# Kernel tuning notes

Measured on AMD Instinct MI355X. Metric: run time of the kernel, lower is better.

Reference implementation:

```python
import jax, jax.numpy as jnp
import numpy as np

N_POINTS = 1_000_000
NUM_PILLARS = 30_000
BN_EPS = 1e-3


def _bn(x, gamma, beta, mean, var):
    # eval-mode BatchNorm1d with eps=0.001
    return (x - mean) * (gamma * jax.lax.rsqrt(var + BN_EPS)) + beta


def setup_inputs() -> dict:
    key = jax.random.key(0)
    ks = jax.random.split(key, 5)
    C1, C2 = 32, 64
    return {
        "points": jax.random.normal(ks[0], (N_POINTS, 5), dtype=jnp.float32),
        "f_center": jax.random.normal(ks[1], (N_POINTS, 3), dtype=jnp.float32),
        "unq_inv": jax.random.randint(ks[2], (N_POINTS,), 0, NUM_PILLARS, dtype=jnp.int32),
        "W1": jax.random.normal(ks[3], (7, C1), dtype=jnp.float32) * 0.1,
        "g1": jnp.ones((C1,), jnp.float32),
        "b1": jnp.zeros((C1,), jnp.float32),
        "m1": jnp.zeros((C1,), jnp.float32),
        "v1": jnp.ones((C1,), jnp.float32),
        "W2": jax.random.normal(ks[4], (C2, C1), dtype=jnp.float32) * 0.1,
        "g2": jnp.ones((C1,), jnp.float32),
        "b2": jnp.zeros((C1,), jnp.float32),
        "m2": jnp.zeros((C1,), jnp.float32),
        "v2": jnp.ones((C1,), jnp.float32),
    }


def reference(points, f_center, unq_inv, W1, g1, b1, m1, v1, W2, g2, b2, m2, v2):
    # gen_feat: concat(f_center, points[:,1:]) -> Linear(no bias) -> BN -> ReLU
    feats = jnp.concatenate([f_center, points[:, 1:]], axis=-1)  # [N, 7]
    h = jnp.maximum(_bn(feats @ W1, g1, b1, m1, v1), 0.0)        # [N, 32]

    # scatter_mean over pillars, then gather back and concat
    seg_sum = jax.ops.segment_sum(h, unq_inv, num_segments=NUM_PILLARS)
    counts = jax.ops.segment_sum(jnp.ones((h.shape[0],), h.dtype), unq_inv,
                                 num_segments=NUM_PILLARS)
    seg_mean = seg_sum / jnp.maximum(counts, 1.0)[:, None]       # [P, 32]
    h2 = jnp.concatenate([h, seg_mean[unq_inv]], axis=1)         # [N, 64]

    # AVFEO: Linear(64,32,no bias) -> BN -> ReLU
    out_fc = jnp.maximum(_bn(h2 @ W2, g2, b2, m2, v2), 0.0)      # [N, 32]

    # scatter_max over pillars (empty pillars -> 0, as torch_scatter)
    seg_max = jax.ops.segment_max(out_fc, unq_inv, num_segments=NUM_PILLARS)
    return jnp.where(jnp.isfinite(seg_max), seg_max, 0.0)        # [P, 32]
```

## Files before the change

kernel.cpp:

```cpp
#include <hip/hip_runtime.h>

typedef __attribute__((ext_vector_type(8))) short short8;
typedef __attribute__((ext_vector_type(4))) float floatx4;

static constexpr float EPS = 1e-3f;

#define CAP8  88
#define NB1   64
#define CCAP  20480
#define FCAP  384

#define P_W1F  0
#define P_B1F  224
#define P_W2L  256
#define P_B2F  1280
#define P_W2UT 1312
#define PREP_F 2048

__device__ __forceinline__ unsigned short f2bf(float x) {
  unsigned u = __float_as_uint(x);
  u += 0x7FFFu + ((u >> 16) & 1u);
  return (unsigned short)(u >> 16);
}

__global__ __launch_bounds__(256)
void k_zero_prep(int* __restrict__ tails,
                 const float* __restrict__ W1, const float* __restrict__ g1,
                 const float* __restrict__ b1, const float* __restrict__ m1,
                 const float* __restrict__ v1,
                 const float* __restrict__ W2, const float* __restrict__ g2,
                 const float* __restrict__ b2, const float* __restrict__ m2,
                 const float* __restrict__ v2, float* __restrict__ prep) {
  const int id = blockIdx.x * 256 + threadIdx.x;
  if (id < 4096) tails[id] = 0;
  if (blockIdx.x == 0) {
    const int t = threadIdx.x;
    for (int i = t; i < 224; i += 256) {
      int c = i & 31;
      prep[P_W1F + i] = W1[i] * (g1[c] * rsqrtf(v1[c] + EPS));
    }
    if (t < 32) {
      float s1 = g1[t] * rsqrtf(v1[t] + EPS);
      float s2 = g2[t] * rsqrtf(v2[t] + EPS);
      prep[P_B1F + t] = b1[t] - m1[t] * s1;
      prep[P_B2F + t] = b2[t] - m2[t] * s2;
    }
    unsigned short* wt = (unsigned short*)(prep + P_W2UT);
    for (int i = t; i < 1024; i += 256) {
      int k = i >> 5, c = i & 31;
      float s2 = g2[c] * rsqrtf(v2[c] + EPS);
      prep[P_W2L + i] = W2[(32 + k) * 32 + c] * s2;
      wt[c * 32 + k] = f2bf(W2[k * 32 + c] * s2);
    }
  }
}

__global__ __launch_bounds__(256)
void k_bin1(const float* __restrict__ points, const float* __restrict__ fc,
            const int* __restrict__ unq, int* __restrict__ tails,
            float* __restrict__ cbuf, int N) {
  __shared__ __align__(16) float4 orec[2048];
  __shared__ int hist[NB1], sbase[NB1], gbase[NB1];
  __shared__ int dst[1024];

  const int t = threadIdx.x;
  const int tile0 = blockIdx.x * 1024;
  const int ntile = min(1024, N - tile0);
  if (t < NB1) hist[t] = 0;
  __syncthreads();

  float4 ra[4], rb[4];
  int bb[4], rr[4];
#pragma unroll
  for (int u = 0; u < 4; ++u) {
    const int j = t + u * 256;
    if (j < ntile) {
      const size_t i = (size_t)tile0 + j;
      float4 a, b;
      a.x = fc[3 * i];     a.y = fc[3 * i + 1]; a.z = fc[3 * i + 2];
      a.w = points[5 * i + 1];
      b.x = points[5 * i + 2]; b.y = points[5 * i + 3]; b.z = points[5 * i + 4];
      const int p = unq[i];
      b.w = __int_as_float(p);
      ra[u] = a; rb[u] = b;
      bb[u] = p >> 9;
      rr[u] = atomicAdd(&hist[bb[u]], 1);
    } else bb[u] = -1;
  }
  __syncthreads();

  if (t < 64) {
    const int h = hist[t];
    int x = h;
    for (int d = 1; d < 64; d <<= 1) {
      int y = __shfl_up(x, d);
      if (t >= d) x += y;
    }
    sbase[t] = x - h;
    gbase[t] = (h > 0) ? atomicAdd(&tails[t], h) : 0;
  }
  __syncthreads();

#pragma unroll
  for (int u = 0; u < 4; ++u) {
    if (bb[u] >= 0) {
      const int s = sbase[bb[u]] + rr[u];
      orec[2 * s] = ra[u];
      orec[2 * s + 1] = rb[u];
      const int gd = gbase[bb[u]] + rr[u];
      dst[s] = (gd < CCAP) ? (bb[u] * CCAP + gd) : -1;
    }
  }
  __syncthreads();

  float4* cb4 = (float4*)cbuf;
  for (int k2 = t; k2 < 2 * ntile; k2 += 256) {
    const int d = dst[k2 >> 1];
    if (d >= 0) cb4[(size_t)d * 2 + (k2 & 1)] = orec[k2];
  }
}

__global__ __launch_bounds__(256)
void k_bin2(const int* __restrict__ tails_ro, int* __restrict__ tails,
            const float* __restrict__ cbuf, float* __restrict__ fgbuf) {
  __shared__ __align__(16) float4 orec[2048];
  __shared__ int hist[64], sbase[64], gbase[64];
  __shared__ int dst[1024];

  const int b = blockIdx.x / 20, tl = blockIdx.x % 20;
  const int n_b = min(tails_ro[b], CCAP);
  const int tile0 = tl * 1024;
  const int ntile = min(1024, n_b - tile0);
  if (ntile <= 0) return;

  const int t = threadIdx.x;
  if (t < 64) hist[t] = 0;
  __syncthreads();

  const float4* src = (const float4*)cbuf + ((size_t)b * CCAP + tile0) * 2;
  float4 ra[4], rb[4];
  int bb[4], rr[4];
#pragma unroll
  for (int u = 0; u < 4; ++u) {
    const int j = t + u * 256;
    if (j < ntile) {
      ra[u] = src[2 * j];
      rb[u] = src[2 * j + 1];
      const int p = __float_as_int(rb[u].w);
      bb[u] = (p >> 3) & 63;
      rr[u] = atomicAdd(&hist[bb[u]], 1);
    } else bb[u] = -1;
  }
  __syncthreads();

  if (t < 64) {
    const int h = hist[t];
    int x = h;
    for (int d = 1; d < 64; d <<= 1) {
      int y = __shfl_up(x, d);
      if (t >= d) x += y;
    }
    sbase[t] = x - h;
    gbase[t] = (h > 0) ? atomicAdd(&tails[64 + (b << 6) + t], h) : 0;
  }
  __syncthreads();

#pragma unroll
  for (int u = 0; u < 4; ++u) {
    if (bb[u] >= 0) {
      const int s = sbase[bb[u]] + rr[u];
      orec[2 * s] = ra[u];
      orec[2 * s + 1] = rb[u];
      const int gd = gbase[bb[u]] + rr[u];
      dst[s] = (gd < FCAP) ? (((b << 6) + bb[u]) * FCAP + gd) : -1;
    }
  }
  __syncthreads();

  float4* fb4 = (float4*)fgbuf;
  for (int k2 = t; k2 < 2 * ntile; k2 += 256) {
    const int d = dst[k2 >> 1];
    if (d >= 0) fb4[(size_t)d * 2 + (k2 & 1)] = orec[k2];
  }
}

__global__ __launch_bounds__(512)
void k_pillar(const float* __restrict__ prep, const int* __restrict__ tails,
              const float* __restrict__ fgbuf, float* __restrict__ out,
              int npil) {
  __shared__ __align__(16) float rec[FCAP][8];
  __shared__ unsigned short ord[8][CAP8];
  __shared__ __align__(16) unsigned short hbuf[8 * CAP8 * 32];
  __shared__ __align__(16) unsigned short w2t[1024];
  __shared__ __align__(16) float sumb[8][32];
  __shared__ int cnt8[8];

  const int t = threadIdx.x;
  if (t < 256) ((uint2*)w2t)[t] = ((const uint2*)(prep + P_W2UT))[t];
  if (t < 8) cnt8[t] = 0;
  __syncthreads();

  const int fb = blockIdx.x;
  const int nrec = min(tails[64 + fb], FCAP);

  const float4* src = (const float4*)(fgbuf + (size_t)fb * FCAP * 8);
  for (int j = t; j < nrec; j += 512) {
    float4 a = src[2 * j], b = src[2 * j + 1];
    ((float4*)rec[j])[0] = a;
    ((float4*)rec[j])[1] = b;
    const int pl = __float_as_int(b.w) & 7;
    const int slot = atomicAdd(&cnt8[pl], 1);
    if (slot < CAP8) ord[pl][slot] = (unsigned short)j;
  }
  __syncthreads();

  const int w = t >> 6, lane = t & 63;
  const int c = lane & 31, half = lane >> 5;
  const int p = fb * 8 + w;
  if (p >= npil) return;
  int n = cnt8[w];
  n = n < CAP8 ? n : CAP8;

  float w1c[7];
#pragma unroll
  for (int r = 0; r < 7; ++r) w1c[r] = prep[P_W1F + r * 32 + c];
  const float b1c = prep[P_B1F + c];
  const float b2c = prep[P_B2F + c];

  float ps = 0.f;
  const int rbase = w * CAP8;
#pragma unroll 2
  for (int s = half; s < n; s += 2) {
    const int j = ord[w][s];
    const floatx4 fa = *(const floatx4*)rec[j];
    const floatx4 fv = *(const floatx4*)(rec[j] + 4);
    float d = fa.x * w1c[0];
    d = fmaf(fa.y, w1c[1], d);
    d = fmaf(fa.z, w1c[2], d);
    d = fmaf(fa.w, w1c[3], d);
    d = fmaf(fv.x, w1c[4], d);
    d = fmaf(fv.y, w1c[5], d);
    d = fmaf(fv.z, w1c[6], d);
    const float h = fmaxf(d + b1c, 0.f);
    ps += h;
    const int row = rbase + s;
    hbuf[row * 32 + (c ^ (((row >> 1) & 3) << 3))] = f2bf(h);
  }
  ps += __shfl_xor(ps, 32);
  if (half == 0) sumb[w][c] = ps;
  __builtin_amdgcn_wave_barrier();

  float acc = 0.f;
  const floatx4* sb4 = (const floatx4*)sumb[w];
#pragma unroll
  for (int kq = 0; kq < 8; ++kq) {
    floatx4 sv = sb4[kq];
    acc = fmaf(sv.x, prep[P_W2L + (kq * 4 + 0) * 32 + c], acc);
    acc = fmaf(sv.y, prep[P_W2L + (kq * 4 + 1) * 32 + c], acc);
    acc = fmaf(sv.z, prep[P_W2L + (kq * 4 + 2) * 32 + c], acc);
    acc = fmaf(sv.w, prep[P_W2L + (kq * 4 + 3) * 32 + c], acc);
  }
  const float inv_n = (n > 0) ? 1.f / (float)n : 1.f;
  const float pc = fmaf(inv_n, acc, b2c);

  const int m16 = lane & 15, q4 = lane >> 4;
  const short8 bf0 = *(const short8*)(w2t + m16 * 32 + q4 * 8);
  const short8 bf1 = *(const short8*)(w2t + (m16 + 16) * 32 + q4 * 8);
  float m0 = -INFINITY, m1 = -INFINITY;
  const int ntiles = (n + 15) >> 4;
  for (int rt = 0; rt < ntiles; ++rt) {
    const int row = rbase + rt * 16 + m16;
    short8 af = *(const short8*)(hbuf + row * 32 +
                                 ((q4 ^ ((row >> 1) & 3)) << 3));
    floatx4 z = {0.f, 0.f, 0.f, 0.f};
    floatx4 a0 = __builtin_amdgcn_mfma_f32_16x16x32_bf16(af, bf0, z, 0, 0, 0);
    floatx4 a1 = __builtin_amdgcn_mfma_f32_16x16x32_bf16(af, bf1, z, 0, 0, 0);
    const int rowb = rt * 16 + q4 * 4;
#pragma unroll
    for (int r = 0; r < 4; ++r) {
      if (rowb + r < n) {
        m0 = fmaxf(m0, a0[r]);
        m1 = fmaxf(m1, a1[r]);
      }
    }
  }
  m0 = fmaxf(m0, __shfl_xor(m0, 16));
  m0 = fmaxf(m0, __shfl_xor(m0, 32));
  m1 = fmaxf(m1, __shfl_xor(m1, 16));
  m1 = fmaxf(m1, __shfl_xor(m1, 32));

  if (lane < 32) {
    float q = (lane & 16) ? m1 : m0;
    out[p * 32 + lane] = fmaxf(q + pc, 0.f);
  }
}

extern "C" void kernel_launch(void* const* d_in, const int* in_sizes, int n_in,
                              void* d_out, int out_size, void* d_ws, size_t ws_size,
                              hipStream_t stream) {
  const float* points = (const float*)d_in[0];
  const float* fc     = (const float*)d_in[1];
  const int*   unq    = (const int*)d_in[2];
  const float* W1 = (const float*)d_in[3];
  const float* g1 = (const float*)d_in[4];
  const float* b1 = (const float*)d_in[5];
  const float* m1 = (const float*)d_in[6];
  const float* v1 = (const float*)d_in[7];
  const float* W2 = (const float*)d_in[8];
  const float* g2 = (const float*)d_in[9];
  const float* b2 = (const float*)d_in[10];
  const float* m2 = (const float*)d_in[11];
  const float* v2 = (const float*)d_in[12];

  const int N    = in_sizes[0] / 5;
  const int NPIL = out_size / 32;

  float* ws = (float*)d_ws;
  int* tails = (int*)ws;
  float* prep = ws + 4096;
  float* cbuf = prep + PREP_F;
  float* fgbuf = cbuf + (size_t)59 * CCAP * 8;

  k_zero_prep<<<16, 256, 0, stream>>>(tails, W1, g1, b1, m1, v1,
                                      W2, g2, b2, m2, v2, prep);

  k_bin1<<<(N + 1023) / 1024, 256, 0, stream>>>(points, fc, unq, tails, cbuf, N);

  k_bin2<<<59 * 20, 256, 0, stream>>>(tails, tails, cbuf, fgbuf);

  const int nfb = (NPIL + 7) / 8;
  k_pillar<<<nfb, 512, 0, stream>>>(prep, tails, fgbuf, (float*)d_out, NPIL);
}
```

Before: 192.8 us.

## Sort compact index/pillar pairs instead of full records, gather rows in pillar kernel

Point features are first packed into a dense 8-float row buffer in a single coalesced pass. The two binning passes then move only (point index, pillar id) int2 pairs instead of 32-byte records, which cuts scatter traffic in both bin kernels. Bin tiles grow to 2048 points with vectorized unq loads. In exchange, the pillar kernel now does a random 32-byte gather per point from the row buffer, and there is an extra full write and read of that buffer.

```diff
diff --git a/kernel.cpp b/kernel.cpp
--- a/kernel.cpp
+++ b/kernel.cpp
@@ -24,15 +24,17 @@
 }
 
 __global__ __launch_bounds__(256)
-void k_zero_prep(int* __restrict__ tails,
+void k_prep_row8(const float* __restrict__ points, const float* __restrict__ fc,
+                 int* __restrict__ tails, float* __restrict__ row8,
                  const float* __restrict__ W1, const float* __restrict__ g1,
                  const float* __restrict__ b1, const float* __restrict__ m1,
                  const float* __restrict__ v1,
                  const float* __restrict__ W2, const float* __restrict__ g2,
                  const float* __restrict__ b2, const float* __restrict__ m2,
-                 const float* __restrict__ v2, float* __restrict__ prep) {
-  const int id = blockIdx.x * 256 + threadIdx.x;
-  if (id < 4096) tails[id] = 0;
+                 const float* __restrict__ v2, float* __restrict__ prep,
+                 int N) {
+  const int gid = blockIdx.x * 256 + threadIdx.x;
+  if (gid < 4096) tails[gid] = 0;
   if (blockIdx.x == 0) {
     const int t = threadIdx.x;
     for (int i = t; i < 224; i += 256) {
@@ -53,39 +55,47 @@
       wt[c * 32 + k] = f2bf(W2[k * 32 + c] * s2);
     }
   }
+  if (gid < N) {
+    const size_t i = (size_t)gid;
+    float4 a, b;
+    a.x = fc[3 * i];     a.y = fc[3 * i + 1]; a.z = fc[3 * i + 2];
+    a.w = points[5 * i + 1];
+    b.x = points[5 * i + 2]; b.y = points[5 * i + 3]; b.z = points[5 * i + 4];
+    b.w = 0.f;
+    float4* dst = (float4*)(row8 + i * 8);
+    dst[0] = a;
+    dst[1] = b;
+  }
 }
 
 __global__ __launch_bounds__(256)
-void k_bin1(const float* __restrict__ points, const float* __restrict__ fc,
-            const int* __restrict__ unq, int* __restrict__ tails,
-            float* __restrict__ cbuf, int N) {
-  __shared__ __align__(16) float4 orec[2048];
+void k_bin1(const int* __restrict__ unq, int* __restrict__ tails,
+            int2* __restrict__ cbuf, int N) {
+  __shared__ int2 orec[2048];
+  __shared__ int dst[2048];
   __shared__ int hist[NB1], sbase[NB1], gbase[NB1];
-  __shared__ int dst[1024];
 
   const int t = threadIdx.x;
-  const int tile0 = blockIdx.x * 1024;
-  const int ntile = min(1024, N - tile0);
+  const int tile0 = blockIdx.x * 2048;
+  const int ntile = min(2048, N - tile0);
   if (t < NB1) hist[t] = 0;
   __syncthreads();
 
-  float4 ra[4], rb[4];
-  int bb[4], rr[4];
-#pragma unroll
-  for (int u = 0; u < 4; ++u) {
-    const int j = t + u * 256;
-    if (j < ntile) {
-      const size_t i = (size_t)tile0 + j;
-      float4 a, b;
-      a.x = fc[3 * i];     a.y = fc[3 * i + 1]; a.z = fc[3 * i + 2];
-      a.w = points[5 * i + 1];
-      b.x = points[5 * i + 2]; b.y = points[5 * i + 3]; b.z = points[5 * i + 4];
-      const int p = unq[i];
-      b.w = __int_as_float(p);
-      ra[u] = a; rb[u] = b;
-      bb[u] = p >> 9;
+  int pv[8], rr[8], bb[8];
+  const int lbase = t * 8;
+  if (lbase < ntile) {
+    const int4* u4 = (const int4*)(unq + tile0 + lbase);
+    int4 ua = u4[0], ub = u4[1];
+    pv[0] = ua.x; pv[1] = ua.y; pv[2] = ua.z; pv[3] = ua.w;
+    pv[4] = ub.x; pv[5] = ub.y; pv[6] = ub.z; pv[7] = ub.w;
+#pragma unroll
+    for (int u = 0; u < 8; ++u) {
+      bb[u] = pv[u] >> 9;
       rr[u] = atomicAdd(&hist[bb[u]], 1);
-    } else bb[u] = -1;
+    }
+  } else {
+#pragma unroll
+    for (int u = 0; u < 8; ++u) bb[u] = -1;
   }
   __syncthreads();
 
@@ -101,53 +111,50 @@
   }
   __syncthreads();
 
-#pragma unroll
-  for (int u = 0; u < 4; ++u) {
-    if (bb[u] >= 0) {
+  if (bb[0] >= 0) {
+#pragma unroll
+    for (int u = 0; u < 8; ++u) {
       const int s = sbase[bb[u]] + rr[u];
-      orec[2 * s] = ra[u];
-      orec[2 * s + 1] = rb[u];
+      orec[s] = make_int2(tile0 + lbase + u, pv[u]);
       const int gd = gbase[bb[u]] + rr[u];
       dst[s] = (gd < CCAP) ? (bb[u] * CCAP + gd) : -1;
     }
   }
   __syncthreads();
 
-  float4* cb4 = (float4*)cbuf;
-  for (int k2 = t; k2 < 2 * ntile; k2 += 256) {
-    const int d = dst[k2 >> 1];
-    if (d >= 0) cb4[(size_t)d * 2 + (k2 & 1)] = orec[k2];
+  for (int k = t; k < ntile; k += 256) {
+    const int d = dst[k];
+    if (d >= 0) cbuf[d] = orec[k];
   }
 }
 
 __global__ __launch_bounds__(256)
 void k_bin2(const int* __restrict__ tails_ro, int* __restrict__ tails,
-            const float* __restrict__ cbuf, float* __restrict__ fgbuf) {
-  __shared__ __align__(16) float4 orec[2048];
+            const int2* __restrict__ cbuf, int2* __restrict__ fgbuf) {
+  __shared__ int2 orec[2048];
+  __shared__ int dst[2048];
   __shared__ int hist[64], sbase[64], gbase[64];
-  __shared__ int dst[1024];
-
-  const int b = blockIdx.x / 20, tl = blockIdx.x % 20;
+
+  const int b = blockIdx.x / 10, tl = blockIdx.x % 10;
   const int n_b = min(tails_ro[b], CCAP);
-  const int tile0 = tl * 1024;
-  const int ntile = min(1024, n_b - tile0);
+  const int tile0 = tl * 2048;
+  const int ntile = min(2048, n_b - tile0);
   if (ntile <= 0) return;
 
   const int t = threadIdx.x;
   if (t < 64) hist[t] = 0;
   __syncthreads();
 
-  const float4* src = (const float4*)cbuf + ((size_t)b * CCAP + tile0) * 2;
-  float4 ra[4], rb[4];
-  int bb[4], rr[4];
-#pragma unroll
-  for (int u = 0; u < 4; ++u) {
-    const int j = t + u * 256;
+  const int2* src = cbuf + (size_t)b * CCAP + tile0;
+  int2 rv[8];
+  int rr[8], bb[8];
+  const int lbase = t * 8;
+#pragma unroll
+  for (int u = 0; u < 8; ++u) {
+    const int j = lbase + u;
     if (j < ntile) {
-      ra[u] = src[2 * j];
-      rb[u] = src[2 * j + 1];
-      const int p = __float_as_int(rb[u].w);
-      bb[u] = (p >> 3) & 63;
+      rv[u] = src[j];
+      bb[u] = (rv[u].y >> 3) & 63;
       rr[u] = atomicAdd(&hist[bb[u]], 1);
     } else bb[u] = -1;
   }
@@ -166,28 +173,26 @@
   __syncthreads();
 
 #pragma unroll
-  for (int u = 0; u < 4; ++u) {
+  for (int u = 0; u < 8; ++u) {
     if (bb[u] >= 0) {
       const int s = sbase[bb[u]] + rr[u];
-      orec[2 * s] = ra[u];
-      orec[2 * s + 1] = rb[u];
+      orec[s] = rv[u];
       const int gd = gbase[bb[u]] + rr[u];
       dst[s] = (gd < FCAP) ? (((b << 6) + bb[u]) * FCAP + gd) : -1;
     }
   }
   __syncthreads();
 
-  float4* fb4 = (float4*)fgbuf;
-  for (int k2 = t; k2 < 2 * ntile; k2 += 256) {
-    const int d = dst[k2 >> 1];
-    if (d >= 0) fb4[(size_t)d * 2 + (k2 & 1)] = orec[k2];
+  for (int k = t; k < ntile; k += 256) {
+    const int d = dst[k];
+    if (d >= 0) fgbuf[d] = orec[k];
   }
 }
 
 __global__ __launch_bounds__(512)
 void k_pillar(const float* __restrict__ prep, const int* __restrict__ tails,
-              const float* __restrict__ fgbuf, float* __restrict__ out,
-              int npil) {
+              const int2* __restrict__ fgbuf, const float* __restrict__ row8,
+              float* __restrict__ out, int npil) {
   __shared__ __align__(16) float rec[FCAP][8];
   __shared__ unsigned short ord[8][CAP8];
   __shared__ __align__(16) unsigned short hbuf[8 * CAP8 * 32];
@@ -203,12 +208,13 @@
   const int fb = blockIdx.x;
   const int nrec = min(tails[64 + fb], FCAP);
 
-  const float4* src = (const float4*)(fgbuf + (size_t)fb * FCAP * 8);
+  const int2* src = fgbuf + (size_t)fb * FCAP;
   for (int j = t; j < nrec; j += 512) {
-    float4 a = src[2 * j], b = src[2 * j + 1];
-    ((float4*)rec[j])[0] = a;
-    ((float4*)rec[j])[1] = b;
-    const int pl = __float_as_int(b.w) & 7;
+    const int2 r = src[j];
+    const floatx4* rp = (const floatx4*)(row8 + (size_t)r.x * 8);
+    ((floatx4*)rec[j])[0] = rp[0];
+    ((floatx4*)rec[j])[1] = rp[1];
+    const int pl = r.y & 7;
     const int slot = atomicAdd(&cnt8[pl], 1);
     if (slot < CAP8) ord[pl][slot] = (unsigned short)j;
   }
@@ -318,16 +324,19 @@
   float* ws = (float*)d_ws;
   int* tails = (int*)ws;
   float* prep = ws + 4096;
-  float* cbuf = prep + PREP_F;
-  float* fgbuf = cbuf + (size_t)59 * CCAP * 8;
-
-  k_zero_prep<<<16, 256, 0, stream>>>(tails, W1, g1, b1, m1, v1,
-                                      W2, g2, b2, m2, v2, prep);
-
-  k_bin1<<<(N + 1023) / 1024, 256, 0, stream>>>(points, fc, unq, tails, cbuf, N);
-
-  k_bin2<<<59 * 20, 256, 0, stream>>>(tails, tails, cbuf, fgbuf);
+  float* row8 = prep + PREP_F;
+  int2* cbuf = (int2*)(row8 + (size_t)N * 8);
+  int2* fgbuf = cbuf + (size_t)59 * CCAP;
+
+  k_prep_row8<<<(N + 255) / 256, 256, 0, stream>>>(points, fc, tails, row8,
+                                                   W1, g1, b1, m1, v1,
+                                                   W2, g2, b2, m2, v2, prep, N);
+
+  k_bin1<<<(N + 2047) / 2048, 256, 0, stream>>>(unq, tails, cbuf, N);
+
+  k_bin2<<<59 * 10, 256, 0, stream>>>(tails, tails, cbuf, fgbuf);
 
   const int nfb = (NPIL + 7) / 8;
-  k_pillar<<<nfb, 512, 0, stream>>>(prep, tails, fgbuf, (float*)d_out, NPIL);
-}
+  k_pillar<<<nfb, 512, 0, stream>>>(prep, tails, fgbuf, row8,
+                                    (float*)d_out, NPIL);
+}
```

After: 167.9 us. 12.9% less time.
